# Optimization experiments

Hardware: AMD Instinct MI355X
Metric: run time of the kernel (lower is better)

Reference implementation:

```python
import jax, jax.numpy as jnp
import numpy as np

B = 8192          # batch of agents
K = 4             # max_neighbors
NUM_LANES = 12
LANE_F = 4        # obs_dim // num_lanes = 48 // 12
HEADS = 4
OUT = 32          # gat_output_dim per head
EMB = HEADS * OUT # 128, gat_per_lane_output / intersection emb dim
HID = 64          # graphsage_hidden_dim
GRU_H = 32        # gru_hidden_dim
ALPHA = 0.2       # leaky relu slope

# Lane cooperation: lanes of the same approach (4 approaches x 3 lanes) cooperate.
_blk = np.kron(np.eye(4), np.ones((3, 3))).astype(np.float32)
LANE_COOP = jnp.asarray(_blk)
LANE_CONF = jnp.asarray(1.0 - _blk)


def _gat_stream(x, W, a_src, a_dst, adj):
    # x: [N, 12, 4]; W: [H, 4, O]; a_*: [H, O]; adj: [12, 12]
    Wh = jnp.einsum('nlf,hfo->nhlo', x, W)                      # [N,H,12,O]
    e_s = jnp.einsum('nhlo,ho->nhl', Wh, a_src)
    e_d = jnp.einsum('nhlo,ho->nhl', Wh, a_dst)
    e = jax.nn.leaky_relu(e_s[..., :, None] + e_d[..., None, :], ALPHA)  # [N,H,12,12]
    e = jnp.where(adj[None, None] > 0, e, jnp.float32(-1e9))
    att = jax.nn.softmax(e, axis=-1)
    out = jnp.einsum('nhij,nhjo->niho', att, Wh)                # [N,12,H,O]
    return jax.nn.elu(out.reshape(out.shape[0], NUM_LANES, EMB))


def _gru_final(xs, Wih, Whh, bih, bhh):
    # xs: [K, B, HID] -> final hidden [B, GRU_H], torch GRU gate convention (r,z,n)
    def step(h, x):
        gi = x @ Wih + bih
        gh = h @ Whh + bhh
        i_r, i_z, i_n = jnp.split(gi, 3, axis=-1)
        h_r, h_z, h_n = jnp.split(gh, 3, axis=-1)
        r = jax.nn.sigmoid(i_r + h_r)
        z = jax.nn.sigmoid(i_z + h_z)
        n = jnp.tanh(i_n + r * h_n)
        return (1.0 - z) * n + z * h, None
    h0 = jnp.zeros((xs.shape[1], Whh.shape[0]), xs.dtype)
    hT, _ = jax.lax.scan(step, h0, xs)
    return hT


def setup_inputs() -> dict:
    key = jax.random.key(0)
    ks = jax.random.split(key, 24)
    rn = lambda k, s: (jax.random.normal(k, s, jnp.float32) * 0.1)
    z = lambda n: jnp.zeros((n,), jnp.float32)
    return {
        'self_features': jax.random.normal(ks[0], (B, 48), jnp.float32),
        'neighbor_features': jax.random.normal(ks[1], (B, K, 48), jnp.float32),
        'neighbor_mask': (jax.random.uniform(ks[2], (B, K)) > 0.25).astype(jnp.float32),
        'neighbor_directions': jax.random.randint(ks[3], (B, K), 0, 4).astype(jnp.float32) * 0.25,
        # dual-stream GAT params
        'W_coop': rn(ks[4], (HEADS, LANE_F, OUT)), 'a_src_coop': rn(ks[5], (HEADS, OUT)), 'a_dst_coop': rn(ks[6], (HEADS, OUT)),
        'W_conf': rn(ks[7], (HEADS, LANE_F, OUT)), 'a_src_conf': rn(ks[8], (HEADS, OUT)), 'a_dst_conf': rn(ks[9], (HEADS, OUT)),
        'W_fuse': rn(ks[10], (2 * EMB, EMB)), 'b_fuse': z(EMB),
        # GraphSAGE neighbor projection (+1 for direction feature)
        'W_proj': rn(ks[11], (EMB + 1, HID)), 'b_proj': z(HID),
        # BiGRU (fwd/bwd), torch layout transposed: Wih [HID,3H], Whh [H,3H]
        'Wih_f': rn(ks[12], (HID, 3 * GRU_H)), 'Whh_f': rn(ks[13], (GRU_H, 3 * GRU_H)), 'bih_f': z(3 * GRU_H), 'bhh_f': z(3 * GRU_H),
        'Wih_b': rn(ks[14], (HID, 3 * GRU_H)), 'Whh_b': rn(ks[15], (GRU_H, 3 * GRU_H)), 'bih_b': z(3 * GRU_H), 'bhh_b': z(3 * GRU_H),
        # combine self + BiGRU summary -> network embedding
        'W_out': rn(ks[16], (EMB + 2 * GRU_H, HID)), 'b_out': z(HID),
    }


def reference(self_features, neighbor_features, neighbor_mask, neighbor_directions,
              W_coop, a_src_coop, a_dst_coop, W_conf, a_src_conf, a_dst_conf,
              W_fuse, b_fuse, W_proj, b_proj,
              Wih_f, Whh_f, bih_f, bhh_f, Wih_b, Whh_b, bih_b, bhh_b,
              W_out, b_out):
    Bc, Kc = neighbor_features.shape[:2]
    # run dual-stream GAT on self + all neighbors in one batch of small lane graphs
    allx = jnp.concatenate([self_features[:, None, :], neighbor_features], axis=1)
    allx = allx.reshape(Bc * (Kc + 1), NUM_LANES, LANE_F)
    coop = _gat_stream(allx, W_coop, a_src_coop, a_dst_coop, LANE_COOP)
    conf = _gat_stream(allx, W_conf, a_src_conf, a_dst_conf, LANE_CONF)
    fused = jax.nn.elu(jnp.concatenate([coop, conf], axis=-1) @ W_fuse + b_fuse)  # [N,12,128]
    emb = fused.mean(axis=1).reshape(Bc, Kc + 1, EMB)  # mean pool over lanes
    self_emb = emb[:, 0]          # [B,128]
    nbr_emb = emb[:, 1:]          # [B,K,128]
    # GraphSAGE projection of neighbors (direction-aware), masked
    nbr_in = jnp.concatenate([nbr_emb, neighbor_directions[..., None]], axis=-1)
    x = jax.nn.relu(nbr_in @ W_proj + b_proj) * neighbor_mask[..., None]  # [B,K,HID]
    xs = jnp.swapaxes(x, 0, 1)    # [K,B,HID]
    h_f = _gru_final(xs, Wih_f, Whh_f, bih_f, bhh_f)
    h_b = _gru_final(xs[::-1], Wih_b, Whh_b, bih_b, bhh_b)
    net = jax.nn.relu(jnp.concatenate([self_emb, h_f, h_b], axis=-1) @ W_out + b_out)  # [B,64]
    return jnp.concatenate([self_emb, net], axis=-1)  # [B,192]
```

## Files before the change

kernel.cpp:

```cpp
#include <hip/hip_runtime.h>
#include <hip/hip_bf16.h>
#include <math.h>

typedef short short8 __attribute__((ext_vector_type(8)));
typedef float f32x4  __attribute__((ext_vector_type(4)));
typedef unsigned short u16x4 __attribute__((ext_vector_type(4)));

__device__ __forceinline__ unsigned short f2b(float f) {
  union { float f; unsigned int u; } x; x.f = f;
  return (unsigned short)((x.u + 0x7FFFu + ((x.u >> 16) & 1u)) >> 16);
}
__device__ __forceinline__ float b2f_u(unsigned short u) {
  union { unsigned int u; float f; } x; x.u = ((unsigned int)u) << 16;
  return x.f;
}
__device__ __forceinline__ unsigned int pkbf(float a, float b) {
  union { __hip_bfloat162 h; unsigned int u; } c;
  c.h = __float22bfloat162_rn(make_float2(a, b));
  return c.u;
}
__device__ __forceinline__ float sigm(float x) { return 1.f / (1.f + __expf(-x)); }
__device__ __forceinline__ float eluf(float v) {
  return v > 0.f ? v : (__expf(v) - 1.f);
}

__global__ __launch_bounds__(256) void prepack_kernel(
    const float* __restrict__ Wf,
    const float* __restrict__ Wc, const float* __restrict__ Wn,
    const float* __restrict__ as_c, const float* __restrict__ ad_c,
    const float* __restrict__ as_n, const float* __restrict__ ad_n,
    const float* __restrict__ Wproj,
    const float* __restrict__ Wih_f, const float* __restrict__ Wih_b,
    const float* __restrict__ Wout,
    const float* __restrict__ Whh_f, const float* __restrict__ Whh_b,
    unsigned short* __restrict__ fragB,
    unsigned short* __restrict__ fragWB,
    float* __restrict__ Wa,
    unsigned short* __restrict__ fragP,
    unsigned short* __restrict__ fragIH,
    unsigned short* __restrict__ fragO,
    unsigned short* __restrict__ fragHH)
{
  int e = blockIdx.x * 256 + threadIdx.x;
  unsigned short tmp[8];
  if (e < 4096) {
    int kb = e >> 9, tile = (e >> 6) & 7, lane = e & 63;
    int n = tile * 16 + (lane & 15);
    int kbase = kb * 32 + (lane >> 4) * 8;
#pragma unroll
    for (int j = 0; j < 8; j++) tmp[j] = f2b(Wf[(kbase + j) * 128 + n]);
    *(short8*)(fragB + e * 8) = *(short8*)tmp;
  } else if (e < 5120) {
    int i = e - 4096;
    int s = i >> 9, tile = (i >> 6) & 7, lane = i & 63;
    int c15 = lane & 15, quad = lane >> 4;
    int n = tile * 16 + c15;
    int h = n >> 5, o = n & 31;
    const float* W = s ? Wn : Wc;
#pragma unroll
    for (int j = 0; j < 8; j++) {
      int k = quad * 8 + j;
      tmp[j] = ((k >> 2) == h) ? f2b(W[h * 128 + (k & 3) * 32 + o])
                               : (unsigned short)0;
    }
    *(short8*)(fragWB + i * 8) = *(short8*)tmp;
  } else if (e < 5184) {
    int i = e - 5120;
    int s = i >> 5, d = (i >> 4) & 1, h = (i >> 2) & 3, f = i & 3;
    const float* W = s ? Wn : Wc;
    const float* a = s ? (d ? ad_n : as_n) : (d ? ad_c : as_c);
    float acc = 0.f;
#pragma unroll
    for (int o = 0; o < 32; o++) acc += W[h * 128 + f * 32 + o] * a[h * 32 + o];
    Wa[i] = acc;
  } else if (e < 6208) {
    int i = e - 5184;
    int kb = i >> 8, nt = (i >> 6) & 3, lane = i & 63;
    int c15 = lane & 15, quad = lane >> 4;
#pragma unroll
    for (int j = 0; j < 8; j++)
      tmp[j] = f2b(Wproj[(kb * 32 + quad * 8 + j) * 64 + nt * 16 + c15]);
    *(short8*)(fragP + i * 8) = *(short8*)tmp;
  } else if (e < 7744) {
    int i = e - 6208;
    int d = (i >= 768), r = i - d * 768;
    int kb = r / 384, nt = (r >> 6) % 6, lane = r & 63;
    int c15 = lane & 15, quad = lane >> 4;
    const float* W = d ? Wih_b : Wih_f;
#pragma unroll
    for (int j = 0; j < 8; j++)
      tmp[j] = f2b(W[(kb * 32 + quad * 8 + j) * 96 + nt * 16 + c15]);
    *(short8*)(fragIH + i * 8) = *(short8*)tmp;
  } else if (e < 9280) {
    int r = e - 7744;
    int kb = r >> 8, nt = (r >> 6) & 3, lane = r & 63;
    int c15 = lane & 15, quad = lane >> 4;
#pragma unroll
    for (int j = 0; j < 8; j++)
      tmp[j] = f2b(Wout[(kb * 32 + quad * 8 + j) * 64 + nt * 16 + c15]);
    *(short8*)(fragO + r * 8) = *(short8*)tmp;
  } else if (e < 10048) {
    int i = e - 9280;
    int d = i / 384, r = i - d * 384;
    int nt = r >> 6, lane = r & 63;
    int c15 = lane & 15, quad = lane >> 4;
    const float* W = d ? Whh_b : Whh_f;
#pragma unroll
    for (int j = 0; j < 8; j++)
      tmp[j] = f2b(W[(quad * 8 + j) * 96 + nt * 16 + c15]);
    *(short8*)(fragHH + i * 8) = *(short8*)tmp;
  }
}

__global__ __launch_bounds__(256) void gat_fuse_kernel(
    const float* __restrict__ self_f, const float* __restrict__ nbr_f,
    const float* __restrict__ Wa,
    const unsigned short* __restrict__ fragWB,
    const unsigned short* __restrict__ fragB,
    const float* __restrict__ b_fuse,
    float* __restrict__ emb)
{
  const int tid = threadIdx.x;
  const int w = tid >> 6, lane = tid & 63, c15 = lane & 15, quad = lane >> 4;
  const int n0 = blockIdx.x * 2;
  const int ws = w & 1;
  const int wn = w >> 1;

  __shared__ __align__(16) float sxf[2][12][4];
  __shared__ float sWa[64];
  __shared__ float sed[2][2][4][12];
  __shared__ __align__(16) unsigned short sA[2][2][16][24];
  __shared__ __align__(16) unsigned short scatb[2][16][268];
  __shared__ float sbias[128];

  if (tid < 128) sbias[tid] = b_fuse[tid];
  if (tid < 64) sWa[tid] = Wa[tid];
  if (tid < 96) {
    int nd = tid / 48, f = tid - nd * 48;
    int nn = n0 + nd, b = nn / 5, slot = nn - b * 5;
    float v = (slot == 0) ? self_f[b * 48 + f]
                          : nbr_f[(b * 4 + slot - 1) * 48 + f];
    sxf[nd][f >> 2][f & 3] = v;
  }
  __syncthreads();

  float es_local = 0.f;
  if (tid < 192) {
    int s = tid / 96, r = tid - s * 96;
    int g = r / 48, r2 = r - g * 48;
    int h = r2 / 12, l = r2 - h * 12;
    float ed = 0.f;
#pragma unroll
    for (int f = 0; f < 4; f++) {
      float xv = sxf[g][l][f];
      es_local += xv * sWa[s * 32 + h * 4 + f];
      ed       += xv * sWa[s * 32 + 16 + h * 4 + f];
    }
    sed[g][s][h][l] = ed;
  }
  __syncthreads();

  if (tid < 192) {
    int s = tid / 96, r = tid - s * 96;
    int g = r / 48, r2 = r - g * 48;
    int h = r2 / 12, i = r2 - h * 12;
    int blk = i / 3;
    float xa0 = 0.f, xa1 = 0.f, xa2 = 0.f, xa3 = 0.f;
    if (s == 0) {
      float ev[3];
      float m = -1e30f;
#pragma unroll
      for (int jj = 0; jj < 3; jj++) {
        float e = es_local + sed[g][0][h][blk * 3 + jj];
        e = e > 0.f ? e : 0.2f * e;
        ev[jj] = e;
        m = fmaxf(m, e);
      }
      float sum = 0.f;
#pragma unroll
      for (int jj = 0; jj < 3; jj++) { ev[jj] = __expf(ev[jj] - m); sum += ev[jj]; }
      float inv = 1.f / sum;
#pragma unroll
      for (int jj = 0; jj < 3; jj++) {
        float aj = ev[jj] * inv;
        f32x4 xj = *(const f32x4*)&sxf[g][blk * 3 + jj][0];
        xa0 += aj * xj[0]; xa1 += aj * xj[1];
        xa2 += aj * xj[2]; xa3 += aj * xj[3];
      }
    } else {
      float ev[9];
      float m = -1e30f;
#pragma unroll
      for (int jj = 0; jj < 9; jj++) {
        int j = jj < blk * 3 ? jj : jj + 3;
        float e = es_local + sed[g][1][h][j];
        e = e > 0.f ? e : 0.2f * e;
        ev[jj] = e;
        m = fmaxf(m, e);
      }
      float sum = 0.f;
#pragma unroll
      for (int jj = 0; jj < 9; jj++) { ev[jj] = __expf(ev[jj] - m); sum += ev[jj]; }
      float inv = 1.f / sum;
#pragma unroll
      for (int jj = 0; jj < 9; jj++) {
        int j = jj < blk * 3 ? jj : jj + 3;
        float aj = ev[jj] * inv;
        f32x4 xj = *(const f32x4*)&sxf[g][j][0];
        xa0 += aj * xj[0]; xa1 += aj * xj[1];
        xa2 += aj * xj[2]; xa3 += aj * xj[3];
      }
    }
    uint2 pk = make_uint2(pkbf(xa0, xa1), pkbf(xa2, xa3));
    *(uint2*)&sA[g][s][i][h * 4] = pk;
  }
  __syncthreads();

  {
    const short8 z8 = {0,0,0,0,0,0,0,0};
    short8 a = z8;
    if (quad < 2) a = *(const short8*)&sA[wn][ws][c15][quad * 8];
#pragma unroll
    for (int tile = 0; tile < 8; tile++) {
      short8 bw = *(const short8*)(fragWB + ((ws * 8 + tile) * 64 + lane) * 8);
      f32x4 c = {0.f, 0.f, 0.f, 0.f};
      c = __builtin_amdgcn_mfma_f32_16x16x32_bf16(a, bw, c, 0, 0, 0);
      if (quad < 3) {
        int co = ws * 128 + tile * 16 + c15;
        unsigned int p01 = pkbf(eluf(c[0]), eluf(c[1]));
        unsigned int p23 = pkbf(eluf(c[2]), eluf(c[3]));
        scatb[wn][quad * 4 + 0][co] = (unsigned short)(p01 & 0xffffu);
        scatb[wn][quad * 4 + 1][co] = (unsigned short)(p01 >> 16);
        scatb[wn][quad * 4 + 2][co] = (unsigned short)(p23 & 0xffffu);
        scatb[wn][quad * 4 + 3][co] = (unsigned short)(p23 >> 16);
      }
    }
  }
  __syncthreads();

  {
    f32x4 acc[2][2];
#pragma unroll
    for (int nd = 0; nd < 2; nd++)
#pragma unroll
      for (int tt = 0; tt < 2; tt++) acc[nd][tt] = (f32x4){0.f,0.f,0.f,0.f};
#pragma unroll
    for (int kb = 0; kb < 8; kb++) {
      short8 a0 = *(const short8*)&scatb[0][c15][kb * 32 + (quad << 3)];
      short8 a1 = *(const short8*)&scatb[1][c15][kb * 32 + (quad << 3)];
#pragma unroll
      for (int tt = 0; tt < 2; tt++) {
        short8 bw = *(const short8*)(fragB + ((kb * 8 + 2 * w + tt) * 64 + lane) * 8);
        acc[0][tt] = __builtin_amdgcn_mfma_f32_16x16x32_bf16(a0, bw, acc[0][tt], 0, 0, 0);
        acc[1][tt] = __builtin_amdgcn_mfma_f32_16x16x32_bf16(a1, bw, acc[1][tt], 0, 0, 0);
      }
    }
    float tot[2][2];
#pragma unroll
    for (int nd = 0; nd < 2; nd++) {
#pragma unroll
      for (int tt = 0; tt < 2; tt++) {
        float p = 0.f;
        if (quad < 3) {
          float bcol = sbias[w * 32 + tt * 16 + c15];
#pragma unroll
          for (int r = 0; r < 4; r++) p += eluf(acc[nd][tt][r] + bcol);
        }
        p += __shfl_xor(p, 16);
        p += __shfl_xor(p, 32);
        tot[nd][tt] = p;
      }
    }
    int ndw = quad >> 1, ttw = quad & 1;
    float val = ndw ? (ttw ? tot[1][1] : tot[1][0])
                    : (ttw ? tot[0][1] : tot[0][0]);
    emb[(n0 + ndw) * 128 + w * 32 + ttw * 16 + c15] = val * (1.f / 12.f);
  }
}

__global__ __launch_bounds__(256) void head_kernel(
    const float* __restrict__ emb,
    const float* __restrict__ maskp, const float* __restrict__ dirsp,
    const float* __restrict__ W_proj, const float* __restrict__ b_proj,
    const unsigned short* __restrict__ fragP,
    const unsigned short* __restrict__ fragIH,
    const unsigned short* __restrict__ fragHH,
    const float* __restrict__ bih_f, const float* __restrict__ bhh_f,
    const float* __restrict__ bih_b, const float* __restrict__ bhh_b,
    const unsigned short* __restrict__ fragO,
    const float* __restrict__ b_out,
    float* __restrict__ out)
{
  const int b8 = blockIdx.x * 8;
  const int tid = threadIdx.x;
  const int w = tid >> 6, lane = tid & 63, c15 = lane & 15, quad = lane >> 4;

  __shared__ __align__(16) unsigned short sX[32][72];
  __shared__ __align__(16) unsigned short sgi[2][32][96];
  __shared__ float sH[2][8][32];
  __shared__ __align__(16) unsigned short sHb[2][16][32];
  __shared__ float sgh[2][8][96];
  __shared__ __align__(16) unsigned short sCat[16][200];
  __shared__ float sPB[128];
  __shared__ float sBI[2][96], sBH[2][96], sBO[64];

  if (tid < 64) { sPB[tid] = b_proj[tid]; sPB[64 + tid] = W_proj[128 * 64 + tid]; sBO[tid] = b_out[tid]; }
  if (tid < 96) { sBI[0][tid] = bih_f[tid]; sBI[1][tid] = bih_b[tid];
                  sBH[0][tid] = bhh_f[tid]; sBH[1][tid] = bhh_b[tid]; }
  {
    unsigned int* hb = (unsigned int*)sHb;
    hb[tid] = 0u; hb[tid + 256] = 0u;
    float* hz = (float*)sH;
    for (int i = tid; i < 512; i += 256) hz[i] = 0.f;
  }
  __syncthreads();

  {
    const int mt = w >> 1;
    const int nt0 = (w & 1) * 2;
    const int sloc = mt * 4 + (c15 >> 2);
    const int nbr  = c15 & 3;
    const float* arow = emb + (((b8 + sloc) * 5) + 1 + nbr) * 128;
    short8 a[4];
#pragma unroll
    for (int kb = 0; kb < 4; kb++) {
      const float* p = arow + kb * 32 + quad * 8;
      f32x4 v0 = *(const f32x4*)p;
      f32x4 v1 = *(const f32x4*)(p + 4);
      unsigned short tmp[8];
      tmp[0]=f2b(v0[0]); tmp[1]=f2b(v0[1]); tmp[2]=f2b(v0[2]); tmp[3]=f2b(v0[3]);
      tmp[4]=f2b(v1[0]); tmp[5]=f2b(v1[1]); tmp[6]=f2b(v1[2]); tmp[7]=f2b(v1[3]);
      a[kb] = *(short8*)tmp;
    }
    f32x4 acc0 = {0.f,0.f,0.f,0.f}, acc1 = acc0;
#pragma unroll
    for (int kb = 0; kb < 4; kb++) {
      short8 b0 = *(const short8*)(fragP + ((kb * 4 + nt0    ) * 64 + lane) * 8);
      short8 b1 = *(const short8*)(fragP + ((kb * 4 + nt0 + 1) * 64 + lane) * 8);
      acc0 = __builtin_amdgcn_mfma_f32_16x16x32_bf16(a[kb], b0, acc0, 0, 0, 0);
      acc1 = __builtin_amdgcn_mfma_f32_16x16x32_bf16(a[kb], b1, acc1, 0, 0, 0);
    }
    const int sE = mt * 4 + quad;
    float dirv[4], maskv[4];
#pragma unroll
    for (int r = 0; r < 4; r++) {
      dirv[r]  = dirsp[(b8 + sE) * 4 + r];
      maskv[r] = maskp[(b8 + sE) * 4 + r];
    }
#pragma unroll
    for (int tt = 0; tt < 2; tt++) {
      f32x4 c = tt ? acc1 : acc0;
      int col = (nt0 + tt) * 16 + c15;
#pragma unroll
      for (int r = 0; r < 4; r++) {
        float v = c[r] + dirv[r] * sPB[64 + col] + sPB[col];
        v = fmaxf(v, 0.f) * maskv[r];
        sX[mt * 16 + quad * 4 + r][col] = f2b(v);
      }
    }
  }
  __syncthreads();

  {
    const int mt = w >> 1;
    const int ntb = (w & 1) * 3;
    short8 a[2];
#pragma unroll
    for (int kb = 0; kb < 2; kb++)
      a[kb] = *(const short8*)&sX[mt * 16 + c15][kb * 32 + quad * 8];
#pragma unroll
    for (int d = 0; d < 2; d++) {
#pragma unroll
      for (int t2 = 0; t2 < 3; t2++) {
        int nt = ntb + t2;
        f32x4 acc = {0.f,0.f,0.f,0.f};
#pragma unroll
        for (int kb = 0; kb < 2; kb++) {
          short8 bb = *(const short8*)(fragIH + ((d * 12 + kb * 6 + nt) * 64 + lane) * 8);
          acc = __builtin_amdgcn_mfma_f32_16x16x32_bf16(a[kb], bb, acc, 0, 0, 0);
        }
        int col = nt * 16 + c15;
        float bi = sBI[d][col];
#pragma unroll
        for (int r = 0; r < 4; r++)
          sgi[d][mt * 16 + quad * 4 + r][col] = f2b(acc[r] + bi);
      }
    }
  }
  __syncthreads();

  {
    const int d_mfma = w >> 1;
    const int nt0 = (w & 1) * 3;
    const int u = tid & 31;
    const int s = (tid >> 5) & 7;
    const int grow = s * 4;
    for (int step = 0; step < 4; step++) {
      short8 a = *(const short8*)&sHb[d_mfma][c15][quad * 8];
#pragma unroll
      for (int t2 = 0; t2 < 3; t2++) {
        short8 bb = *(const short8*)(fragHH + ((d_mfma * 6 + nt0 + t2) * 64 + lane) * 8);
        f32x4 c = {0.f,0.f,0.f,0.f};
        c = __builtin_amdgcn_mfma_f32_16x16x32_bf16(a, bb, c, 0, 0, 0);
        if (quad < 2) {
          int col = (nt0 + t2) * 16 + c15;
#pragma unroll
          for (int r = 0; r < 4; r++)
            sgh[d_mfma][quad * 4 + r][col] = c[r];
        }
      }
      __syncthreads();
#pragma unroll
      for (int d = 0; d < 2; d++) {
        int k = d ? (3 - step) : step;
        int row = grow + k;
        float ghr = sgh[d][s][u]      + sBH[d][u];
        float ghz = sgh[d][s][32 + u] + sBH[d][32 + u];
        float ghn = sgh[d][s][64 + u] + sBH[d][64 + u];
        float r = sigm(b2f_u(sgi[d][row][u]) + ghr);
        float z = sigm(b2f_u(sgi[d][row][32 + u]) + ghz);
        float n = tanhf(b2f_u(sgi[d][row][64 + u]) + r * ghn);
        float h = (1.f - z) * n + z * sH[d][s][u];
        sH[d][s][u] = h;
        sHb[d][s][u] = f2b(h);
      }
      __syncthreads();
    }
  }

  for (int i = tid; i < 8 * 128; i += 256) {
    int s = i >> 7, cc = i & 127;
    sCat[s][cc] = f2b(emb[(b8 + s) * 5 * 128 + cc]);
  }
  for (int i = tid; i < 512; i += 256) {
    int s = i >> 6, j = i & 63;
    float hv = (j < 32) ? sH[0][s][j] : sH[1][s][j - 32];
    sCat[s][128 + j] = f2b(hv);
  }
  __syncthreads();

  {
    const int nt = w;
    f32x4 acc = {0.f,0.f,0.f,0.f};
#pragma unroll
    for (int kb = 0; kb < 6; kb++) {
      short8 a = *(const short8*)&sCat[c15][kb * 32 + quad * 8];
      short8 bb = *(const short8*)(fragO + ((kb * 4 + nt) * 64 + lane) * 8);
      acc = __builtin_amdgcn_mfma_f32_16x16x32_bf16(a, bb, acc, 0, 0, 0);
    }
    if (quad < 2) {
      int col = nt * 16 + c15;
#pragma unroll
      for (int r = 0; r < 4; r++) {
        int m = quad * 4 + r;
        out[(b8 + m) * 192 + 128 + col] = fmaxf(acc[r] + sBO[col], 0.f);
      }
    }
  }
  for (int i = tid; i < 8 * 128; i += 256) {
    int s = i >> 7, cc = i & 127;
    out[(b8 + s) * 192 + cc] = emb[(b8 + s) * 5 * 128 + cc];
  }
}

extern "C" void kernel_launch(void* const* d_in, const int* in_sizes, int n_in,
                              void* d_out, int out_size, void* d_ws, size_t ws_size,
                              hipStream_t stream) {
  const float* self_f  = (const float*)d_in[0];
  const float* nbr_f   = (const float*)d_in[1];
  const float* maskp   = (const float*)d_in[2];
  const float* dirsp   = (const float*)d_in[3];
  const float* W_coop  = (const float*)d_in[4];
  const float* as_coop = (const float*)d_in[5];
  const float* ad_coop = (const float*)d_in[6];
  const float* W_conf  = (const float*)d_in[7];
  const float* as_conf = (const float*)d_in[8];
  const float* ad_conf = (const float*)d_in[9];
  const float* W_fuse  = (const float*)d_in[10];
  const float* b_fuse  = (const float*)d_in[11];
  const float* W_proj  = (const float*)d_in[12];
  const float* b_proj  = (const float*)d_in[13];
  const float* Wih_f   = (const float*)d_in[14];
  const float* Whh_f   = (const float*)d_in[15];
  const float* bih_f   = (const float*)d_in[16];
  const float* bhh_f   = (const float*)d_in[17];
  const float* Wih_b   = (const float*)d_in[18];
  const float* Whh_b   = (const float*)d_in[19];
  const float* bih_b   = (const float*)d_in[20];
  const float* bhh_b   = (const float*)d_in[21];
  const float* W_out   = (const float*)d_in[22];
  const float* b_out   = (const float*)d_in[23];

  const int B = in_sizes[0] / 48;
  char* ws = (char*)d_ws;
  unsigned short* fragB  = (unsigned short*)(ws);
  unsigned short* fragWB = (unsigned short*)(ws + 65536);
  float*          Wa     = (float*)(ws + 81920);
  unsigned short* fragP  = (unsigned short*)(ws + 82176);
  unsigned short* fragIH = (unsigned short*)(ws + 98560);
  unsigned short* fragO  = (unsigned short*)(ws + 123136);
  unsigned short* fragHH = (unsigned short*)(ws + 147712);
  float*          emb    = (float*)(ws + 160000);

  prepack_kernel<<<40, 256, 0, stream>>>(
      W_fuse, W_coop, W_conf, as_coop, ad_coop, as_conf, ad_conf,
      W_proj, Wih_f, Wih_b, W_out, Whh_f, Whh_b,
      fragB, fragWB, Wa, fragP, fragIH, fragO, fragHH);

  gat_fuse_kernel<<<B * 5 / 2, 256, 0, stream>>>(
      self_f, nbr_f, Wa, fragWB, fragB, b_fuse, emb);

  head_kernel<<<B / 8, 256, 0, stream>>>(
      emb, maskp, dirsp, W_proj, b_proj, fragP, fragIH, fragHH,
      bih_f, bhh_f, bih_b, bhh_b,
      fragO, b_out, (float*)d_out);
}
```

Before: 234.2 us.

## Remove block barriers by giving each wave its own GAT and GRU work

In the GAT kernel, the attention-logit and softmax phases now run inside a single wave. Each wave handles one (node, stream) pair and writes the sA data it later reads itself, which removes two block-wide barriers. In the tail kernel, the GRU recurrence now runs on two waves, one per direction, with no __syncthreads per step. The other two waves copy the self embedding into both sCat and the output at the same time. This trades cross-wave barrier cost for less parallelism in the GRU step and relies on intra-wave LDS ordering being correct.

```diff
diff --git a/kernel.cpp b/kernel.cpp
--- a/kernel.cpp
+++ b/kernel.cpp
@@ -123,8 +123,6 @@
   const int tid = threadIdx.x;
   const int w = tid >> 6, lane = tid & 63, c15 = lane & 15, quad = lane >> 4;
   const int n0 = blockIdx.x * 2;
-  const int ws = w & 1;
-  const int wn = w >> 1;
 
   __shared__ __align__(16) float sxf[2][12][4];
   __shared__ float sWa[64];
@@ -144,34 +142,25 @@
   }
   __syncthreads();
 
-  float es_local = 0.f;
-  if (tid < 192) {
-    int s = tid / 96, r = tid - s * 96;
-    int g = r / 48, r2 = r - g * 48;
-    int h = r2 / 12, l = r2 - h * 12;
-    float ed = 0.f;
+  const int g_q = w & 1, s_q = w >> 1;
+  if (lane < 48) {
+    int h = lane / 12, i = lane - h * 12;
+    float es = 0.f, ed = 0.f;
 #pragma unroll
     for (int f = 0; f < 4; f++) {
-      float xv = sxf[g][l][f];
-      es_local += xv * sWa[s * 32 + h * 4 + f];
-      ed       += xv * sWa[s * 32 + 16 + h * 4 + f];
-    }
-    sed[g][s][h][l] = ed;
-  }
-  __syncthreads();
-
-  if (tid < 192) {
-    int s = tid / 96, r = tid - s * 96;
-    int g = r / 48, r2 = r - g * 48;
-    int h = r2 / 12, i = r2 - h * 12;
+      float xv = sxf[g_q][i][f];
+      es += xv * sWa[s_q * 32 + h * 4 + f];
+      ed += xv * sWa[s_q * 32 + 16 + h * 4 + f];
+    }
+    sed[g_q][s_q][h][i] = ed;
     int blk = i / 3;
     float xa0 = 0.f, xa1 = 0.f, xa2 = 0.f, xa3 = 0.f;
-    if (s == 0) {
+    if (s_q == 0) {
       float ev[3];
       float m = -1e30f;
 #pragma unroll
       for (int jj = 0; jj < 3; jj++) {
-        float e = es_local + sed[g][0][h][blk * 3 + jj];
+        float e = es + sed[g_q][0][h][blk * 3 + jj];
         e = e > 0.f ? e : 0.2f * e;
         ev[jj] = e;
         m = fmaxf(m, e);
@@ -183,7 +172,7 @@
 #pragma unroll
       for (int jj = 0; jj < 3; jj++) {
         float aj = ev[jj] * inv;
-        f32x4 xj = *(const f32x4*)&sxf[g][blk * 3 + jj][0];
+        f32x4 xj = *(const f32x4*)&sxf[g_q][blk * 3 + jj][0];
         xa0 += aj * xj[0]; xa1 += aj * xj[1];
         xa2 += aj * xj[2]; xa3 += aj * xj[3];
       }
@@ -193,7 +182,7 @@
 #pragma unroll
       for (int jj = 0; jj < 9; jj++) {
         int j = jj < blk * 3 ? jj : jj + 3;
-        float e = es_local + sed[g][1][h][j];
+        float e = es + sed[g_q][1][h][j];
         e = e > 0.f ? e : 0.2f * e;
         ev[jj] = e;
         m = fmaxf(m, e);
@@ -206,33 +195,33 @@
       for (int jj = 0; jj < 9; jj++) {
         int j = jj < blk * 3 ? jj : jj + 3;
         float aj = ev[jj] * inv;
-        f32x4 xj = *(const f32x4*)&sxf[g][j][0];
+        f32x4 xj = *(const f32x4*)&sxf[g_q][j][0];
         xa0 += aj * xj[0]; xa1 += aj * xj[1];
         xa2 += aj * xj[2]; xa3 += aj * xj[3];
       }
     }
     uint2 pk = make_uint2(pkbf(xa0, xa1), pkbf(xa2, xa3));
-    *(uint2*)&sA[g][s][i][h * 4] = pk;
-  }
-  __syncthreads();
-
-  {
+    *(uint2*)&sA[g_q][s_q][i][h * 4] = pk;
+  }
+
+  {
+    const int wn3 = w & 1, ws3 = w >> 1;
     const short8 z8 = {0,0,0,0,0,0,0,0};
     short8 a = z8;
-    if (quad < 2) a = *(const short8*)&sA[wn][ws][c15][quad * 8];
+    if (quad < 2) a = *(const short8*)&sA[wn3][ws3][c15][quad * 8];
 #pragma unroll
     for (int tile = 0; tile < 8; tile++) {
-      short8 bw = *(const short8*)(fragWB + ((ws * 8 + tile) * 64 + lane) * 8);
+      short8 bw = *(const short8*)(fragWB + ((ws3 * 8 + tile) * 64 + lane) * 8);
       f32x4 c = {0.f, 0.f, 0.f, 0.f};
       c = __builtin_amdgcn_mfma_f32_16x16x32_bf16(a, bw, c, 0, 0, 0);
       if (quad < 3) {
-        int co = ws * 128 + tile * 16 + c15;
+        int co = ws3 * 128 + tile * 16 + c15;
         unsigned int p01 = pkbf(eluf(c[0]), eluf(c[1]));
         unsigned int p23 = pkbf(eluf(c[2]), eluf(c[3]));
-        scatb[wn][quad * 4 + 0][co] = (unsigned short)(p01 & 0xffffu);
-        scatb[wn][quad * 4 + 1][co] = (unsigned short)(p01 >> 16);
-        scatb[wn][quad * 4 + 2][co] = (unsigned short)(p23 & 0xffffu);
-        scatb[wn][quad * 4 + 3][co] = (unsigned short)(p23 >> 16);
+        scatb[wn3][quad * 4 + 0][co] = (unsigned short)(p01 & 0xffffu);
+        scatb[wn3][quad * 4 + 1][co] = (unsigned short)(p01 >> 16);
+        scatb[wn3][quad * 4 + 2][co] = (unsigned short)(p23 & 0xffffu);
+        scatb[wn3][quad * 4 + 3][co] = (unsigned short)(p23 >> 16);
       }
     }
   }
@@ -389,31 +378,27 @@
   }
   __syncthreads();
 
-  {
-    const int d_mfma = w >> 1;
-    const int nt0 = (w & 1) * 3;
-    const int u = tid & 31;
-    const int s = (tid >> 5) & 7;
-    const int grow = s * 4;
+  if (w < 2) {
+    const int d = w;
+    const int u = lane & 31, sp = lane >> 5;
     for (int step = 0; step < 4; step++) {
-      short8 a = *(const short8*)&sHb[d_mfma][c15][quad * 8];
-#pragma unroll
-      for (int t2 = 0; t2 < 3; t2++) {
-        short8 bb = *(const short8*)(fragHH + ((d_mfma * 6 + nt0 + t2) * 64 + lane) * 8);
+      short8 a = *(const short8*)&sHb[d][c15][quad * 8];
+#pragma unroll
+      for (int nt = 0; nt < 6; nt++) {
+        short8 bb = *(const short8*)(fragHH + ((d * 6 + nt) * 64 + lane) * 8);
         f32x4 c = {0.f,0.f,0.f,0.f};
         c = __builtin_amdgcn_mfma_f32_16x16x32_bf16(a, bb, c, 0, 0, 0);
         if (quad < 2) {
-          int col = (nt0 + t2) * 16 + c15;
-#pragma unroll
-          for (int r = 0; r < 4; r++)
-            sgh[d_mfma][quad * 4 + r][col] = c[r];
+          int col = nt * 16 + c15;
+#pragma unroll
+          for (int r = 0; r < 4; r++) sgh[d][quad * 4 + r][col] = c[r];
         }
       }
-      __syncthreads();
-#pragma unroll
-      for (int d = 0; d < 2; d++) {
-        int k = d ? (3 - step) : step;
-        int row = grow + k;
+      const int k = d ? (3 - step) : step;
+#pragma unroll
+      for (int si = 0; si < 4; si++) {
+        int s = sp + si * 2;
+        int row = s * 4 + k;
         float ghr = sgh[d][s][u]      + sBH[d][u];
         float ghz = sgh[d][s][32 + u] + sBH[d][32 + u];
         float ghn = sgh[d][s][64 + u] + sBH[d][64 + u];
@@ -423,19 +408,16 @@
         float h = (1.f - z) * n + z * sH[d][s][u];
         sH[d][s][u] = h;
         sHb[d][s][u] = f2b(h);
-      }
-      __syncthreads();
-    }
-  }
-
-  for (int i = tid; i < 8 * 128; i += 256) {
-    int s = i >> 7, cc = i & 127;
-    sCat[s][cc] = f2b(emb[(b8 + s) * 5 * 128 + cc]);
-  }
-  for (int i = tid; i < 512; i += 256) {
-    int s = i >> 6, j = i & 63;
-    float hv = (j < 32) ? sH[0][s][j] : sH[1][s][j - 32];
-    sCat[s][128 + j] = f2b(hv);
+        if (step == 3) sCat[s][128 + d * 32 + u] = f2b(h);
+      }
+    }
+  } else {
+    for (int i = tid - 128; i < 1024; i += 128) {
+      int s = i >> 7, cc = i & 127;
+      float v = emb[(b8 + s) * 5 * 128 + cc];
+      sCat[s][cc] = f2b(v);
+      out[(b8 + s) * 192 + cc] = v;
+    }
   }
   __syncthreads();
 
@@ -456,10 +438,6 @@
         out[(b8 + m) * 192 + 128 + col] = fmaxf(acc[r] + sBO[col], 0.f);
       }
     }
-  }
-  for (int i = tid; i < 8 * 128; i += 256) {
-    int s = i >> 7, cc = i & 127;
-    out[(b8 + s) * 192 + cc] = emb[(b8 + s) * 5 * 128 + cc];
   }
 }
 
```

New measurement: 224.6 us. -4.1%, faster.
